# Kernel tuning notes

Measured on AMD Instinct MI355X. Metric: run time of the kernel, lower is better.

The kernel has to match this reference:

```python
import jax, jax.numpy as jnp
import numpy as np

H, D = 4, 64          # n_heads, feats_per_head (hidden_size = H*D = 256)
NEG_SLOPE = 0.2       # DGL GATv2Conv default negative_slope

N_GT, N_UBS, N_AG = 100000, 20000, 20000
E_SEEN, E_NEAR = 320000, 160000
F_GT, F_UBS, F_AG = 8, 8, 16
HID = H * D


def _linear_params(key, fan_in, fan_out):
    kw, kb = jax.random.split(key)
    s = 1.0 / np.sqrt(fan_in)
    W = jax.random.uniform(kw, (fan_in, fan_out), jnp.float32, -s, s)
    b = jax.random.uniform(kb, (fan_out,), jnp.float32, -s, s)
    return W, b


def setup_inputs() -> dict:
    key = jax.random.key(0)
    ks = jax.random.split(key, 16)
    inp = {
        'x_gt': jax.random.normal(ks[0], (N_GT, F_GT), jnp.float32),
        'x_ubs': jax.random.normal(ks[1], (N_UBS, F_UBS), jnp.float32),
        'x_agent': jax.random.normal(ks[2], (N_AG, F_AG), jnp.float32),
        'seen_src': jax.random.randint(ks[3], (E_SEEN,), 0, N_GT, jnp.int32),
        'seen_dst': jax.random.randint(ks[4], (E_SEEN,), 0, N_AG, jnp.int32),
        'near_src': jax.random.randint(ks[5], (E_NEAR,), 0, N_UBS, jnp.int32),
        'near_dst': jax.random.randint(ks[6], (E_NEAR,), 0, N_AG, jnp.int32),
    }
    # GATv2Conv 'seen': (gt -> agent)
    inp['Ws_seen'], inp['bs_seen'] = _linear_params(ks[7], F_GT, HID)
    inp['Wd_seen'], inp['bd_seen'] = _linear_params(ks[8], F_AG, HID)
    inp['attn_seen'] = jax.random.normal(ks[9], (H, D), jnp.float32) * 0.1
    inp['Wr_seen'], inp['br_seen'] = _linear_params(ks[10], F_AG, HID)
    # GATv2Conv 'near': (ubs -> agent)
    inp['Ws_near'], inp['bs_near'] = _linear_params(ks[11], F_UBS, HID)
    inp['Wd_near'], inp['bd_near'] = _linear_params(ks[12], F_AG, HID)
    inp['attn_near'] = jax.random.normal(ks[13], (H, D), jnp.float32) * 0.1
    inp['Wr_near'], inp['br_near'] = _linear_params(ks[14], F_AG, HID)
    # aggregation MLP: Linear(2*HID, HID) + ReLU
    inp['W_aggr'], inp['b_aggr'] = _linear_params(ks[15], 2 * HID, HID)
    return inp


def _gatv2(h_src, h_dst, src, dst, Ws, bs, Wd, bd, attn, Wr, br, n_dst):
    # DGL GATv2Conv, bipartite, residual=True, allow_zero_in_degree, ReLU activation
    fs = (h_src @ Ws + bs).reshape(-1, H, D)   # [Ns,H,D]
    fd = (h_dst @ Wd + bd).reshape(-1, H, D)   # [Nd,H,D]
    e = jax.nn.leaky_relu(fs[src] + fd[dst], NEG_SLOPE)     # [E,H,D]
    scores = jnp.einsum('ehd,hd->eh', e, attn)              # [E,H]
    # edge softmax over incoming edges of each dst node
    m = jax.ops.segment_max(scores, dst, num_segments=n_dst)
    m = jnp.where(jnp.isfinite(m), m, 0.0)                  # zero-in-degree guard
    ex = jnp.exp(scores - m[dst])
    denom = jax.ops.segment_sum(ex, dst, num_segments=n_dst)
    alpha = ex / denom[dst]                                 # [E,H]
    rst = jax.ops.segment_sum(alpha[:, :, None] * fs[src], dst, num_segments=n_dst)
    rst = rst + (h_dst @ Wr + br).reshape(-1, H, D)         # residual
    return jax.nn.relu(rst).reshape(n_dst, H * D)


def reference(x_gt, x_ubs, x_agent, seen_src, seen_dst, near_src, near_dst,
              Ws_seen, bs_seen, Wd_seen, bd_seen, attn_seen, Wr_seen, br_seen,
              Ws_near, bs_near, Wd_near, bd_near, attn_near, Wr_near, br_near,
              W_aggr, b_aggr):
    n_ag = x_agent.shape[0]
    x1 = _gatv2(x_gt, x_agent, seen_src, seen_dst,
                Ws_seen, bs_seen, Wd_seen, bd_seen, attn_seen, Wr_seen, br_seen, n_ag)
    x2 = _gatv2(x_ubs, x_agent, near_src, near_dst,
                Ws_near, bs_near, Wd_near, bd_near, attn_near, Wr_near, br_near, n_ag)
    x_out = jnp.concatenate((x1, x2), axis=1)               # [N_ag, 2*HID]
    return jax.nn.relu(x_out @ W_aggr + b_aggr)             # [N_ag, HID]
```

## Files before the change

kernel.cpp:

```cpp
#include <hip/hip_runtime.h>
#include <math.h>

#define NEG 0.2f
#define LDSW 520

typedef short bf16x8 __attribute__((ext_vector_type(8)));
typedef float f32x4  __attribute__((ext_vector_type(4)));
typedef float f32x2  __attribute__((ext_vector_type(2)));

static __device__ __forceinline__ f32x2 pkfma(f32x2 a, f32x2 b, f32x2 c) {
    return __builtin_elementwise_fma(a, b, c);
}
static __device__ __forceinline__ f32x2 splat2(float x) { return (f32x2){x, x}; }

static __device__ __forceinline__ unsigned short f2bf(float f) {
    unsigned int x = __float_as_uint(f);
    unsigned int r = (x + 0x7FFFu + ((x >> 16) & 1u)) >> 16;
    return (unsigned short)r;
}
static __device__ __forceinline__ float rlane(float v, int l) {
    return __int_as_float(__builtin_amdgcn_readlane(__float_as_int(v), l));
}

#define DPP_ADD(x, ctrl) \
    ((x) + __int_as_float(__builtin_amdgcn_update_dpp( \
        __float_as_int(x), __float_as_int(x), (ctrl), 0xF, 0xF, true)))
static __device__ __forceinline__ float rowsum16(float v) {
    v = DPP_ADD(v, 0xB1);
    v = DPP_ADD(v, 0x4E);
    v = DPP_ADD(v, 0x141);
    v = DPP_ADD(v, 0x140);
    return v;
}

__global__ void k_hist_wt(const int* __restrict__ dst_s, int Es,
                          const int* __restrict__ dst_n, int En,
                          int* __restrict__ deg_s, int* __restrict__ deg_n,
                          const float* __restrict__ W, unsigned short* __restrict__ Wt) {
    int i = blockIdx.x * 256 + threadIdx.x;
    if (i < Es) atomicAdd(&deg_s[dst_s[i]], 1);
    int j = i - Es;
    if (j >= 0 && j < En) atomicAdd(&deg_n[dst_n[j]], 1);
    if (i < 512 * 256) {
        int k = i >> 8, n = i & 255;
        Wt[(size_t)n * 512 + k] = f2bf(W[i]);
    }
}

__global__ __launch_bounds__(1024) void k_scan2(int* a, int na, int* b, int nb) {
    int* p = (blockIdx.x == 0) ? a : b;
    int n  = (blockIdx.x == 0) ? na : nb;
    __shared__ int sums[1024];
    int t = threadIdx.x;
    int C = (n + 1023) >> 10;
    int base = t * C;
    int s = 0;
    for (int j = 0; j < C; ++j) { int i = base + j; if (i < n) s += p[i]; }
    sums[t] = s;
    __syncthreads();
    for (int off = 1; off < 1024; off <<= 1) {
        int v = (t >= off) ? sums[t - off] : 0;
        __syncthreads();
        sums[t] += v;
        __syncthreads();
    }
    int run = (t == 0) ? 0 : sums[t - 1];
    for (int j = 0; j < C; ++j) {
        int i = base + j;
        if (i < n) { int v = p[i]; p[i] = run; run += v; }
    }
}

__global__ void k_scatter(const int* __restrict__ src_s, const int* __restrict__ dst_s, int Es,
                          const int* __restrict__ src_n, const int* __restrict__ dst_n, int En,
                          int* __restrict__ cur_s, int* __restrict__ cur_n,
                          int* __restrict__ csr_s, int* __restrict__ csr_n) {
    int i = blockIdx.x * 256 + threadIdx.x;
    if (i < Es) {
        int pos = atomicAdd(&cur_s[dst_s[i]], 1);
        csr_s[pos] = src_s[i];
    }
    int j = i - Es;
    if (j >= 0 && j < En) {
        int pos = atomicAdd(&cur_n[dst_n[j]], 1);
        csr_n[pos] = src_n[j];
    }
}

#define EDGE_BODY { \
    f32x2 x0 = splat2(rlane(r0, j * 8 + 0)); \
    f32x2 x1 = splat2(rlane(r0, j * 8 + 1)); \
    f32x2 x2 = splat2(rlane(r0, j * 8 + 2)); \
    f32x2 x3 = splat2(rlane(r0, j * 8 + 3)); \
    f32x2 x4 = splat2(rlane(r0, j * 8 + 4)); \
    f32x2 x5 = splat2(rlane(r0, j * 8 + 5)); \
    f32x2 x6 = splat2(rlane(r0, j * 8 + 6)); \
    f32x2 x7 = splat2(rlane(r0, j * 8 + 7)); \
    f32x2 fs01 = bs01, fs23 = bs23; \
    fs01 = pkfma(x0, ws01[0], fs01); fs23 = pkfma(x0, ws23[0], fs23); \
    fs01 = pkfma(x1, ws01[1], fs01); fs23 = pkfma(x1, ws23[1], fs23); \
    fs01 = pkfma(x2, ws01[2], fs01); fs23 = pkfma(x2, ws23[2], fs23); \
    fs01 = pkfma(x3, ws01[3], fs01); fs23 = pkfma(x3, ws23[3], fs23); \
    fs01 = pkfma(x4, ws01[4], fs01); fs23 = pkfma(x4, ws23[4], fs23); \
    fs01 = pkfma(x5, ws01[5], fs01); fs23 = pkfma(x5, ws23[5], fs23); \
    fs01 = pkfma(x6, ws01[6], fs01); fs23 = pkfma(x6, ws23[6], fs23); \
    fs01 = pkfma(x7, ws01[7], fs01); fs23 = pkfma(x7, ws23[7], fs23); \
    f32x2 t01 = fs01 + fd01r; \
    f32x2 t23 = fs23 + fd23r; \
    t01 = __builtin_elementwise_max(t01, NEG * t01); \
    t23 = __builtin_elementwise_max(t23, NEG * t23); \
    f32x2 scp = t01 * at01; \
    scp = pkfma(t23, at23, scp); \
    float sc = scp.x + scp.y; \
    sc = rowsum16(sc); \
    float p = __expf(sc);    \
    l += p; \
    f32x2 pp = splat2(p); \
    a01 = pkfma(pp, fs01, a01); \
    a23 = pkfma(pp, fs23, a23); }

static __device__ __forceinline__ void gat_layer(
    const float* __restrict__ x_src, const int* __restrict__ csr,
    const float* __restrict__ Ws, const float* __restrict__ bs,
    const float* __restrict__ Wd, const float* __restrict__ bd,
    const float* __restrict__ at,
    const float* __restrict__ Wr, const float* __restrict__ br,
    float xag, int lane,
    const int* st, const int* dg,
    const int* i1pre, const float* x0pre,
    unsigned short* __restrict__ ldsout)
{
    const int d0 = lane * 4;
    const int gs = lane >> 3;
    const int w8 = lane & 7;

    f32x2 fd01[2], fd23[2], fr01[2], fr23[2];
    {
        float4 bdv = *(const float4*)&bd[d0];
        float4 brv = *(const float4*)&br[d0];
#pragma unroll
        for (int j = 0; j < 2; ++j) {
            fd01[j] = (f32x2){bdv.x, bdv.y}; fd23[j] = (f32x2){bdv.z, bdv.w};
            fr01[j] = (f32x2){brv.x, brv.y}; fr23[j] = (f32x2){brv.z, brv.w};
        }
#pragma unroll
        for (int k = 0; k < 16; ++k) {
            float4 wd = *(const float4*)&Wd[k * 256 + d0];
            float4 wr = *(const float4*)&Wr[k * 256 + d0];
            f32x2 wd01 = {wd.x, wd.y}, wd23 = {wd.z, wd.w};
            f32x2 wr01 = {wr.x, wr.y}, wr23 = {wr.z, wr.w};
#pragma unroll
            for (int j = 0; j < 2; ++j) {
                f32x2 xk = splat2(rlane(xag, j * 16 + k));
                fd01[j] = pkfma(xk, wd01, fd01[j]);
                fd23[j] = pkfma(xk, wd23, fd23[j]);
                fr01[j] = pkfma(xk, wr01, fr01[j]);
                fr23[j] = pkfma(xk, wr23, fr23[j]);
            }
        }
    }

    f32x2 ws01[8], ws23[8];
#pragma unroll
    for (int k = 0; k < 8; ++k) {
        float4 w = *(const float4*)&Ws[k * 256 + d0];
        ws01[k] = (f32x2){w.x, w.y};
        ws23[k] = (f32x2){w.z, w.w};
    }
    f32x2 bs01, bs23, at01, at23;
    {
        float4 b4 = *(const float4*)&bs[d0];
        float4 a4 = *(const float4*)&at[d0];
        bs01 = (f32x2){b4.x, b4.y}; bs23 = (f32x2){b4.z, b4.w};
        at01 = (f32x2){a4.x, a4.y}; at23 = (f32x2){a4.z, a4.w};
    }

#pragma unroll
    for (int rep = 0; rep < 2; ++rep) {
        const int start = st[rep];
        const int deg   = dg[rep];
        const f32x2 fd01r = fd01[rep], fd23r = fd23[rep];

        float l = 0.f;
        f32x2 a01 = {0.f, 0.f}, a23 = {0.f, 0.f};

        if (deg > 0) {
            float r0 = x0pre[rep];
            int   i1 = i1pre[rep];
            const int nfull = deg >> 3, tail = deg & 7;

            for (int c = 0; c < nfull; ++c) {
                float r1 = x_src[(size_t)i1 * 8 + w8];
                int e2 = c * 8 + 16 + gs; e2 = (e2 < deg) ? e2 : deg - 1;
                int i2 = csr[start + e2];
#pragma unroll
                for (int j = 0; j < 8; ++j) EDGE_BODY
                r0 = r1; i1 = i2;
            }
            if (tail) {
#pragma unroll
                for (int j = 0; j < 8; ++j)
                    if (j < tail) EDGE_BODY
            }
        }

        float inv = (l > 0.f) ? 1.f / l : 0.f;
        ushort4 o;
        o.x = f2bf(fmaxf(fmaf(a01.x, inv, fr01[rep].x), 0.f));
        o.y = f2bf(fmaxf(fmaf(a01.y, inv, fr01[rep].y), 0.f));
        o.z = f2bf(fmaxf(fmaf(a23.x, inv, fr23[rep].x), 0.f));
        o.w = f2bf(fmaxf(fmaf(a23.y, inv, fr23[rep].y), 0.f));
        *(ushort4*)(ldsout + rep * LDSW) = o;
    }
}

__global__ __launch_bounds__(512) void k_gatmlp(
    const float* __restrict__ xsrc_s, const int* __restrict__ pfx_s, const int* __restrict__ csr_s,
    const float* __restrict__ Ws_s, const float* __restrict__ bs_s,
    const float* __restrict__ Wd_s, const float* __restrict__ bd_s,
    const float* __restrict__ at_s,
    const float* __restrict__ Wr_s, const float* __restrict__ br_s,
    const float* __restrict__ xsrc_n, const int* __restrict__ pfx_n, const int* __restrict__ csr_n,
    const float* __restrict__ Ws_n, const float* __restrict__ bs_n,
    const float* __restrict__ Wd_n, const float* __restrict__ bd_n,
    const float* __restrict__ at_n,
    const float* __restrict__ Wr_n, const float* __restrict__ br_n,
    const float* __restrict__ x_ag,
    const unsigned short* __restrict__ Wt, const float* __restrict__ bmlp,
    float* __restrict__ out, int n_dst)
{
    __shared__ unsigned short xt[16 * LDSW];

    const int t = threadIdx.x;
    const int wave = t >> 6, lane = t & 63;
    const int gs = lane >> 3, w8 = lane & 7;
    const int nb = (int)blockIdx.x * 16;

    int nd0 = nb + wave * 2;     nd0 = (nd0 < n_dst) ? nd0 : n_dst - 1;
    int nd1 = nb + wave * 2 + 1; nd1 = (nd1 < n_dst) ? nd1 : n_dst - 1;

    float xag = x_ag[(size_t)(((lane >> 4) & 1) ? nd1 : nd0) * 16 + (lane & 15)];

    int stS[2], dgS[2], stN[2], dgN[2];
#pragma unroll
    for (int j = 0; j < 2; ++j) {
        int n = j ? nd1 : nd0;
        int eS = pfx_s[n], sS = n ? pfx_s[n - 1] : 0;
        int eN = pfx_n[n], sN = n ? pfx_n[n - 1] : 0;
        stS[j] = sS; dgS[j] = eS - sS;
        stN[j] = sN; dgN[j] = eN - sN;
    }

    int i0S[2], i1S[2]; float x0S[2];
#pragma unroll
    for (int j = 0; j < 2; ++j) {
        int dgj = dgS[j];
        if (dgj > 0) {
            int e0 = (gs < dgj) ? gs : dgj - 1;
            int e1 = (8 + gs < dgj) ? 8 + gs : dgj - 1;
            i0S[j] = csr_s[stS[j] + e0];
            i1S[j] = csr_s[stS[j] + e1];
        } else { i0S[j] = 0; i1S[j] = 0; }
    }
#pragma unroll
    for (int j = 0; j < 2; ++j)
        x0S[j] = xsrc_s[(size_t)i0S[j] * 8 + w8];

    unsigned short* ldsA = &xt[(wave * 2) * LDSW + lane * 4];
    gat_layer(xsrc_s, csr_s, Ws_s, bs_s, Wd_s, bd_s, at_s, Wr_s, br_s,
              xag, lane, stS, dgS, i1S, x0S, ldsA);

    int i0N[2], i1N[2]; float x0N[2];
#pragma unroll
    for (int j = 0; j < 2; ++j) {
        int dgj = dgN[j];
        if (dgj > 0) {
            int e0 = (gs < dgj) ? gs : dgj - 1;
            int e1 = (8 + gs < dgj) ? 8 + gs : dgj - 1;
            i0N[j] = csr_n[stN[j] + e0];
            i1N[j] = csr_n[stN[j] + e1];
        } else { i0N[j] = 0; i1N[j] = 0; }
    }
#pragma unroll
    for (int j = 0; j < 2; ++j)
        x0N[j] = xsrc_n[(size_t)i0N[j] * 8 + w8];

    gat_layer(xsrc_n, csr_n, Ws_n, bs_n, Wd_n, bd_n, at_n, Wr_n, br_n,
              xag, lane, stN, dgN, i1N, x0N, ldsA + 256);

    __syncthreads();

    const int m16 = lane & 15, q = lane >> 4;
    const unsigned short* w0 = Wt + (size_t)(wave * 32 + m16) * 512 + q * 8;
    const unsigned short* w1 = w0 + 16 * 512;
    const unsigned short* ap = &xt[m16 * LDSW + q * 8];

    f32x4 ac0 = {0.f, 0.f, 0.f, 0.f}, ac1 = ac0;
#pragma unroll
    for (int k0 = 0; k0 < 512; k0 += 32) {
        bf16x8 a  = *(const bf16x8*)(ap + k0);
        bf16x8 b0 = *(const bf16x8*)(w0 + k0);
        bf16x8 b1 = *(const bf16x8*)(w1 + k0);
        ac0 = __builtin_amdgcn_mfma_f32_16x16x32_bf16(a, b0, ac0, 0, 0, 0);
        ac1 = __builtin_amdgcn_mfma_f32_16x16x32_bf16(a, b1, ac1, 0, 0, 0);
    }

#define EPI(AC, J) { \
        int coln = wave * 32 + (J) * 16 + m16; \
        float bv = bmlp[coln]; \
        _Pragma("unroll") \
        for (int r = 0; r < 4; ++r) { \
            int orow = nb + q * 4 + r; \
            if (orow < n_dst) \
                out[(size_t)orow * 256 + coln] = fmaxf(AC[r] + bv, 0.f); \
        } }
    EPI(ac0, 0) EPI(ac1, 1)
#undef EPI
}

extern "C" void kernel_launch(void* const* d_in, const int* in_sizes, int n_in,
                              void* d_out, int out_size, void* d_ws, size_t ws_size,
                              hipStream_t stream) {
    const float* x_gt   = (const float*)d_in[0];
    const float* x_ubs  = (const float*)d_in[1];
    const float* x_ag   = (const float*)d_in[2];
    const int* seen_src = (const int*)d_in[3];
    const int* seen_dst = (const int*)d_in[4];
    const int* near_src = (const int*)d_in[5];
    const int* near_dst = (const int*)d_in[6];
    const float* Ws_s = (const float*)d_in[7];  const float* bs_s = (const float*)d_in[8];
    const float* Wd_s = (const float*)d_in[9];  const float* bd_s = (const float*)d_in[10];
    const float* at_s = (const float*)d_in[11];
    const float* Wr_s = (const float*)d_in[12]; const float* br_s = (const float*)d_in[13];
    const float* Ws_n = (const float*)d_in[14]; const float* bs_n = (const float*)d_in[15];
    const float* Wd_n = (const float*)d_in[16]; const float* bd_n = (const float*)d_in[17];
    const float* at_n = (const float*)d_in[18];
    const float* Wr_n = (const float*)d_in[19]; const float* br_n = (const float*)d_in[20];
    const float* W_a  = (const float*)d_in[21]; const float* b_a  = (const float*)d_in[22];

    const int n_ag = in_sizes[2] / 16;
    const int E_s  = in_sizes[3];
    const int E_n  = in_sizes[5];

    char* ws = (char*)d_ws;
    int* cur_s = (int*)ws;              ws += (size_t)n_ag * 4;
    int* cur_n = (int*)ws;              ws += (size_t)n_ag * 4;
    int* csr_s = (int*)ws;              ws += (size_t)E_s * 4;
    int* csr_n = (int*)ws;              ws += (size_t)E_n * 4;
    unsigned short* Wt   = (unsigned short*)ws;

    hipMemsetAsync(cur_s, 0, (size_t)n_ag * 8, stream);

    int gE = (E_s + E_n + 255) / 256;
    k_hist_wt<<<gE, 256, 0, stream>>>(seen_dst, E_s, near_dst, E_n, cur_s, cur_n, W_a, Wt);
    k_scan2<<<2, 1024, 0, stream>>>(cur_s, n_ag, cur_n, n_ag);
    k_scatter<<<gE, 256, 0, stream>>>(seen_src, seen_dst, E_s, near_src, near_dst, E_n,
                                      cur_s, cur_n, csr_s, csr_n);

    int gN = (n_ag + 15) / 16;
    k_gatmlp<<<gN, 512, 0, stream>>>(
        x_gt,  cur_s, csr_s, Ws_s, bs_s, Wd_s, bd_s, at_s, Wr_s, br_s,
        x_ubs, cur_n, csr_n, Ws_n, bs_n, Wd_n, bd_n, at_n, Wr_n, br_n,
        x_ag, Wt, b_a, (float*)d_out, n_ag);
}
```

Baseline: 311.1 us.

## Halve block to 4 waves, each handling 4 destination nodes and 64 MLP columns

The fused GAT+MLP kernel now launches 256 threads per 16-node block instead of 512. Each wave processes 4 destination nodes per GAT layer instead of 2, which spreads the per-wave Wd/Wr/Ws weight loads and projections over more nodes. In the MLP stage each wave computes 64 output columns with four MFMA accumulators. This lowers thread count and weight reloads per node but raises register pressure and serialises more edge loops within each wave. Node-to-wave mapping is interleaved and out-of-range nodes are skipped.

New measurement: 339.5 us. +9.1%, slower.

```diff
diff --git a/kernel.cpp b/kernel.cpp
--- a/kernel.cpp
+++ b/kernel.cpp
@@ -119,27 +119,27 @@
     a01 = pkfma(pp, fs01, a01); \
     a23 = pkfma(pp, fs23, a23); }
 
-static __device__ __forceinline__ void gat_layer(
+static __device__ __forceinline__ void gat_layer4(
     const float* __restrict__ x_src, const int* __restrict__ csr,
     const float* __restrict__ Ws, const float* __restrict__ bs,
     const float* __restrict__ Wd, const float* __restrict__ bd,
     const float* __restrict__ at,
     const float* __restrict__ Wr, const float* __restrict__ br,
-    float xag, int lane,
+    float xag, int lane, int wave, int nb, int n_dst,
     const int* st, const int* dg,
     const int* i1pre, const float* x0pre,
-    unsigned short* __restrict__ ldsout)
+    unsigned short* __restrict__ ldsbase)
 {
     const int d0 = lane * 4;
     const int gs = lane >> 3;
     const int w8 = lane & 7;
 
-    f32x2 fd01[2], fd23[2], fr01[2], fr23[2];
+    f32x2 fd01[4], fd23[4], fr01[4], fr23[4];
     {
         float4 bdv = *(const float4*)&bd[d0];
         float4 brv = *(const float4*)&br[d0];
 #pragma unroll
-        for (int j = 0; j < 2; ++j) {
+        for (int j = 0; j < 4; ++j) {
             fd01[j] = (f32x2){bdv.x, bdv.y}; fd23[j] = (f32x2){bdv.z, bdv.w};
             fr01[j] = (f32x2){brv.x, brv.y}; fr23[j] = (f32x2){brv.z, brv.w};
         }
@@ -150,7 +150,7 @@
             f32x2 wd01 = {wd.x, wd.y}, wd23 = {wd.z, wd.w};
             f32x2 wr01 = {wr.x, wr.y}, wr23 = {wr.z, wr.w};
 #pragma unroll
-            for (int j = 0; j < 2; ++j) {
+            for (int j = 0; j < 4; ++j) {
                 f32x2 xk = splat2(rlane(xag, j * 16 + k));
                 fd01[j] = pkfma(xk, wd01, fd01[j]);
                 fd23[j] = pkfma(xk, wd23, fd23[j]);
@@ -176,7 +176,10 @@
     }
 
 #pragma unroll
-    for (int rep = 0; rep < 2; ++rep) {
+    for (int rep = 0; rep < 4; ++rep) {
+        const int node = nb + rep * 4 + wave;
+        if (node >= n_dst) continue;
+
         const int start = st[rep];
         const int deg   = dg[rep];
         const f32x2 fd01r = fd01[rep], fd23r = fd23[rep];
@@ -210,11 +213,11 @@
         o.y = f2bf(fmaxf(fmaf(a01.y, inv, fr01[rep].y), 0.f));
         o.z = f2bf(fmaxf(fmaf(a23.x, inv, fr23[rep].x), 0.f));
         o.w = f2bf(fmaxf(fmaf(a23.y, inv, fr23[rep].y), 0.f));
-        *(ushort4*)(ldsout + rep * LDSW) = o;
-    }
-}
-
-__global__ __launch_bounds__(512) void k_gatmlp(
+        *(ushort4*)(ldsbase + (rep * 4 + wave) * LDSW) = o;
+    }
+}
+
+__global__ __launch_bounds__(256) void k_gatmlp(
     const float* __restrict__ xsrc_s, const int* __restrict__ pfx_s, const int* __restrict__ csr_s,
     const float* __restrict__ Ws_s, const float* __restrict__ bs_s,
     const float* __restrict__ Wd_s, const float* __restrict__ bd_s,
@@ -236,24 +239,24 @@
     const int gs = lane >> 3, w8 = lane & 7;
     const int nb = (int)blockIdx.x * 16;
 
-    int nd0 = nb + wave * 2;     nd0 = (nd0 < n_dst) ? nd0 : n_dst - 1;
-    int nd1 = nb + wave * 2 + 1; nd1 = (nd1 < n_dst) ? nd1 : n_dst - 1;
-
-    float xag = x_ag[(size_t)(((lane >> 4) & 1) ? nd1 : nd0) * 16 + (lane & 15)];
-
-    int stS[2], dgS[2], stN[2], dgN[2];
-#pragma unroll
-    for (int j = 0; j < 2; ++j) {
-        int n = j ? nd1 : nd0;
-        int eS = pfx_s[n], sS = n ? pfx_s[n - 1] : 0;
-        int eN = pfx_n[n], sN = n ? pfx_n[n - 1] : 0;
+    int gnode = nb + ((lane >> 4) << 2) + wave;
+    int gn = (gnode < n_dst) ? gnode : (n_dst - 1);
+    float xag = x_ag[(size_t)gn * 16 + (lane & 15)];
+
+    int stS[4], dgS[4], stN[4], dgN[4];
+#pragma unroll
+    for (int j = 0; j < 4; ++j) {
+        int nd = nb + j * 4 + wave;
+        nd = (nd < n_dst) ? nd : (n_dst - 1);
+        int eS = pfx_s[nd], sS = nd ? pfx_s[nd - 1] : 0;
+        int eN = pfx_n[nd], sN = nd ? pfx_n[nd - 1] : 0;
         stS[j] = sS; dgS[j] = eS - sS;
         stN[j] = sN; dgN[j] = eN - sN;
     }
 
-    int i0S[2], i1S[2]; float x0S[2];
-#pragma unroll
-    for (int j = 0; j < 2; ++j) {
+    int i0S[4], i1S[4], i0N[4], i1N[4];
+#pragma unroll
+    for (int j = 0; j < 4; ++j) {
         int dgj = dgS[j];
         if (dgj > 0) {
             int e0 = (gs < dgj) ? gs : dgj - 1;
@@ -263,16 +266,7 @@
         } else { i0S[j] = 0; i1S[j] = 0; }
     }
 #pragma unroll
-    for (int j = 0; j < 2; ++j)
-        x0S[j] = xsrc_s[(size_t)i0S[j] * 8 + w8];
-
-    unsigned short* ldsA = &xt[(wave * 2) * LDSW + lane * 4];
-    gat_layer(xsrc_s, csr_s, Ws_s, bs_s, Wd_s, bd_s, at_s, Wr_s, br_s,
-              xag, lane, stS, dgS, i1S, x0S, ldsA);
-
-    int i0N[2], i1N[2]; float x0N[2];
-#pragma unroll
-    for (int j = 0; j < 2; ++j) {
+    for (int j = 0; j < 4; ++j) {
         int dgj = dgN[j];
         if (dgj > 0) {
             int e0 = (gs < dgj) ? gs : dgj - 1;
@@ -281,32 +275,49 @@
             i1N[j] = csr_n[stN[j] + e1];
         } else { i0N[j] = 0; i1N[j] = 0; }
     }
-#pragma unroll
-    for (int j = 0; j < 2; ++j)
+    float x0S[4];
+#pragma unroll
+    for (int j = 0; j < 4; ++j)
+        x0S[j] = xsrc_s[(size_t)i0S[j] * 8 + w8];
+
+    unsigned short* ldsbase = &xt[lane * 4];
+    gat_layer4(xsrc_s, csr_s, Ws_s, bs_s, Wd_s, bd_s, at_s, Wr_s, br_s,
+               xag, lane, wave, nb, n_dst, stS, dgS, i1S, x0S, ldsbase);
+
+    float x0N[4];
+#pragma unroll
+    for (int j = 0; j < 4; ++j)
         x0N[j] = xsrc_n[(size_t)i0N[j] * 8 + w8];
 
-    gat_layer(xsrc_n, csr_n, Ws_n, bs_n, Wd_n, bd_n, at_n, Wr_n, br_n,
-              xag, lane, stN, dgN, i1N, x0N, ldsA + 256);
+    gat_layer4(xsrc_n, csr_n, Ws_n, bs_n, Wd_n, bd_n, at_n, Wr_n, br_n,
+               xag, lane, wave, nb, n_dst, stN, dgN, i1N, x0N, ldsbase + 256);
 
     __syncthreads();
 
     const int m16 = lane & 15, q = lane >> 4;
-    const unsigned short* w0 = Wt + (size_t)(wave * 32 + m16) * 512 + q * 8;
+    const int nbase = wave * 64;
+    const unsigned short* w0 = Wt + (size_t)(nbase + m16) * 512 + q * 8;
     const unsigned short* w1 = w0 + 16 * 512;
+    const unsigned short* w2 = w0 + 32 * 512;
+    const unsigned short* w3 = w0 + 48 * 512;
     const unsigned short* ap = &xt[m16 * LDSW + q * 8];
 
-    f32x4 ac0 = {0.f, 0.f, 0.f, 0.f}, ac1 = ac0;
+    f32x4 ac0 = {0.f, 0.f, 0.f, 0.f}, ac1 = ac0, ac2 = ac0, ac3 = ac0;
 #pragma unroll
     for (int k0 = 0; k0 < 512; k0 += 32) {
         bf16x8 a  = *(const bf16x8*)(ap + k0);
         bf16x8 b0 = *(const bf16x8*)(w0 + k0);
         bf16x8 b1 = *(const bf16x8*)(w1 + k0);
+        bf16x8 b2 = *(const bf16x8*)(w2 + k0);
+        bf16x8 b3 = *(const bf16x8*)(w3 + k0);
         ac0 = __builtin_amdgcn_mfma_f32_16x16x32_bf16(a, b0, ac0, 0, 0, 0);
         ac1 = __builtin_amdgcn_mfma_f32_16x16x32_bf16(a, b1, ac1, 0, 0, 0);
+        ac2 = __builtin_amdgcn_mfma_f32_16x16x32_bf16(a, b2, ac2, 0, 0, 0);
+        ac3 = __builtin_amdgcn_mfma_f32_16x16x32_bf16(a, b3, ac3, 0, 0, 0);
     }
 
 #define EPI(AC, J) { \
-        int coln = wave * 32 + (J) * 16 + m16; \
+        int coln = nbase + (J) * 16 + m16; \
         float bv = bmlp[coln]; \
         _Pragma("unroll") \
         for (int r = 0; r < 4; ++r) { \
@@ -314,7 +325,7 @@
             if (orow < n_dst) \
                 out[(size_t)orow * 256 + coln] = fmaxf(AC[r] + bv, 0.f); \
         } }
-    EPI(ac0, 0) EPI(ac1, 1)
+    EPI(ac0, 0) EPI(ac1, 1) EPI(ac2, 2) EPI(ac3, 3)
 #undef EPI
 }
 
@@ -358,7 +369,7 @@
                                       cur_s, cur_n, csr_s, csr_n);
 
     int gN = (n_ag + 15) / 16;
-    k_gatmlp<<<gN, 512, 0, stream>>>(
+    k_gatmlp<<<gN, 256, 0, stream>>>(
         x_gt,  cur_s, csr_s, Ws_s, bs_s, Wd_s, bd_s, at_s, Wr_s, br_s,
         x_ubs, cur_n, csr_n, Ws_n, bs_n, Wd_n, bd_n, at_n, Wr_n, br_n,
         x_ag, Wt, b_a, (float*)d_out, n_ag);
```
